# Kernel optimization log

Hardware: AMD Instinct MI355X
Metric: run time of the kernel (lower is better)

Reference implementation:

```python
import jax, jax.numpy as jnp
import numpy as np

N_NODES = 100000
N_EDGES = 3200000
IN_C, HID_C, OUT_C = 5, 128, 64


def setup_inputs() -> dict:
    key = jax.random.key(0)
    k_x, k_e, k_w1, k_b1, k_w2, k_b2 = jax.random.split(key, 6)
    x = jax.random.normal(k_x, (N_NODES, IN_C), dtype=jnp.float32)
    edge_index = jax.random.randint(k_e, (2, N_EDGES), 0, N_NODES, dtype=jnp.int32)
    # GCNConv learned params (glorot weights, zero-ish bias)
    W1 = jax.random.normal(k_w1, (IN_C, HID_C), dtype=jnp.float32) * (1.0 / np.sqrt(IN_C))
    b1 = jax.random.normal(k_b1, (HID_C,), dtype=jnp.float32) * 0.01
    W2 = jax.random.normal(k_w2, (HID_C, OUT_C), dtype=jnp.float32) * (1.0 / np.sqrt(HID_C))
    b2 = jax.random.normal(k_b2, (OUT_C,), dtype=jnp.float32) * 0.01
    return {"x": x, "edge_index": edge_index, "W1": W1, "b1": b1, "W2": W2, "b2": b2}


def _gcn_conv(x, src, dst, deg_inv_sqrt, W, b):
    """One GCNConv (PyG defaults: self-loops already in src/dst, symmetric norm, bias)."""
    h = x @ W                                   # [N, C_out]
    norm = deg_inv_sqrt[src] * deg_inv_sqrt[dst]  # [E+N]
    msg = h[src] * norm[:, None]                # gather + scale
    out = jax.ops.segment_sum(msg, dst, num_segments=x.shape[0])  # scatter-add
    return out + b


def reference(x, edge_index, W1, b1, W2, b2):
    n = x.shape[0]
    loop = jnp.arange(n, dtype=edge_index.dtype)
    src = jnp.concatenate([edge_index[0], loop])  # self-loops appended
    dst = jnp.concatenate([edge_index[1], loop])
    deg = jax.ops.segment_sum(jnp.ones_like(src, dtype=x.dtype), dst, num_segments=n)
    deg_inv_sqrt = jnp.where(deg > 0, jax.lax.rsqrt(deg), 0.0)
    h = _gcn_conv(x, src, dst, deg_inv_sqrt, W1, b1)
    z = _gcn_conv(h, src, dst, deg_inv_sqrt, W2, b2)
    return z
```

## Files before the change

### kernel.cpp

```cpp
#include <hip/hip_runtime.h>

#define IN_C  5
#define HID_C 128
#define OUT_C 64

#define KB   256
#define NBP  512
#define CAP  10240
#define TILE 4096
#define BTH  512
#define EPT  (TILE / BTH)
#define GNODES 64


__global__ void k_init(int* __restrict__ gcursor) {
    gcursor[threadIdx.x] = threadIdx.x * CAP;
}

__global__ __launch_bounds__(BTH) void k_bin(const int* __restrict__ src,
                                             const int* __restrict__ dstp,
                                             int* __restrict__ gcursor,
                                             int* __restrict__ binned, int e) {
    __shared__ int lhist[NBP];
    __shared__ int lfill[NBP];
    __shared__ int lgpos[NBP];
    int tid = threadIdx.x;
    int tbeg = blockIdx.x * TILE;
    for (int j = tid; j < NBP; j += BTH) { lhist[j] = 0; lfill[j] = 0; }
    __syncthreads();
    int pk[EPT], bk[EPT];
    #pragma unroll
    for (int q = 0; q < EPT; ++q) {
        int idx = tbeg + q * BTH + tid;
        if (idx < e) {
            int s = src[idx], d = dstp[idx];
            pk[q] = ((d & 255) << 24) | s;
            bk[q] = ((unsigned)d) >> 8;
            atomicAdd(&lhist[bk[q]], 1);
        } else bk[q] = -1;
    }
    __syncthreads();
    int hv = lhist[tid];
    if (hv > 0) lgpos[tid] = atomicAdd(&gcursor[tid], hv);
    __syncthreads();
    #pragma unroll
    for (int q = 0; q < EPT; ++q) {
        if (bk[q] >= 0) {
            int pos = lgpos[bk[q]] + atomicAdd(&lfill[bk[q]], 1);
            binned[pos] = pk[q];
        }
    }
}

__global__ __launch_bounds__(BTH) void k_build(int* __restrict__ binned,
                                               const int* __restrict__ gcursor,
                                               const float* __restrict__ x,
                                               int2* __restrict__ pse,
                                               float* __restrict__ xs, int n) {
    __shared__ int cnt[KB];
    __shared__ int wt[4];
    __shared__ int wte[4];
    __shared__ int stage[CAP];
    int tid = threadIdx.x;
    int lane = tid & 63, w = tid >> 6;
    int bkt = blockIdx.x;
    int beg = bkt * CAP;
    int tot = gcursor[bkt] - beg;
    if (tid < KB) cnt[tid] = 0;
    __syncthreads();
    int4 r[5];
    #pragma unroll
    for (int it = 0; it < 5; ++it) {
        int j0 = (tid << 2) + it * (BTH * 4);
        if (j0 < tot) {
            r[it] = *(const int4*)(binned + beg + j0);
            atomicAdd(&cnt[((unsigned)r[it].x) >> 24], 1);
            if (j0 + 1 < tot) atomicAdd(&cnt[((unsigned)r[it].y) >> 24], 1);
            if (j0 + 2 < tot) atomicAdd(&cnt[((unsigned)r[it].z) >> 24], 1);
            if (j0 + 3 < tot) atomicAdd(&cnt[((unsigned)r[it].w) >> 24], 1);
        }
    }
    __syncthreads();
    int deg = (tid < KB) ? cnt[tid] : 0;
    int v = deg;
    #pragma unroll
    for (int m = 1; m < 64; m <<= 1) { int u = __shfl_up(v, m); if (lane >= m) v += u; }
    if (tid < KB && lane == 63) wt[w] = v;
    __syncthreads();
    if (tid == 0) {
        int s = 0;
        #pragma unroll
        for (int k = 0; k < 4; ++k) { wte[k] = s; s += wt[k]; }
    }
    __syncthreads();
    if (tid < KB) {
        int rel = wte[w] + v - deg;
        int node = bkt * KB + tid;
        pse[node] = make_int2(beg + rel, beg + rel + deg);
        cnt[tid] = rel;
        float d = rsqrtf(1.0f + (float)deg);
        float4 q0 = {0, 0, 0, 0}, q1 = {0, 0, 0, 0};
        if (node < n) {
            q0.x = x[node * IN_C + 0] * d;
            q0.y = x[node * IN_C + 1] * d;
            q0.z = x[node * IN_C + 2] * d;
            q0.w = x[node * IN_C + 3] * d;
            q1.x = x[node * IN_C + 4] * d;
            q1.y = d;
        }
        ((float4*)(xs + (size_t)node * 8))[0] = q0;
        ((float4*)(xs + (size_t)node * 8))[1] = q1;
    }
    __syncthreads();
    #pragma unroll
    for (int it = 0; it < 5; ++it) {
        int j0 = (tid << 2) + it * (BTH * 4);
        if (j0 < tot) {
            {
                int slot = atomicAdd(&cnt[((unsigned)r[it].x) >> 24], 1);
                stage[slot] = r[it].x & 0xFFFFFF;
            }
            if (j0 + 1 < tot) {
                int slot = atomicAdd(&cnt[((unsigned)r[it].y) >> 24], 1);
                stage[slot] = r[it].y & 0xFFFFFF;
            }
            if (j0 + 2 < tot) {
                int slot = atomicAdd(&cnt[((unsigned)r[it].z) >> 24], 1);
                stage[slot] = r[it].z & 0xFFFFFF;
            }
            if (j0 + 3 < tot) {
                int slot = atomicAdd(&cnt[((unsigned)r[it].w) >> 24], 1);
                stage[slot] = r[it].w & 0xFFFFFF;
            }
        }
    }
    __syncthreads();
    for (int j = tid; j < tot; j += BTH)
        binned[beg + j] = stage[j];
}

__global__ __launch_bounds__(BTH) void k_gath0(const int* __restrict__ srclist,
                                               const int2* __restrict__ pse,
                                               const float* __restrict__ feat,
                                               float* __restrict__ outf,
                                               float* __restrict__ tout, int n) {
    int tid = threadIdx.x;
    int node = blockIdx.x * GNODES + (tid >> 3);
    int sub = tid & 7;
    if (node >= n) return;
    int2 pp = pse[node];
    int ps = pp.x, pe = pp.y;
    float a0 = 0, a1 = 0, a2 = 0, a3 = 0, a4 = 0, a5 = 0;
    int j = ps + sub;
    for (; j + 24 < pe; j += 32) {
        int s0 = srclist[j],      s1 = srclist[j + 8];
        int s2 = srclist[j + 16], s3 = srclist[j + 24];
        const float4* q0 = (const float4*)(feat + (size_t)s0 * 8);
        const float4* q1 = (const float4*)(feat + (size_t)s1 * 8);
        const float4* q2 = (const float4*)(feat + (size_t)s2 * 8);
        const float4* q3 = (const float4*)(feat + (size_t)s3 * 8);
        float4 rA0 = q0[0], rA1 = q0[1];
        float4 rB0 = q1[0], rB1 = q1[1];
        float4 rC0 = q2[0], rC1 = q2[1];
        float4 rD0 = q3[0], rD1 = q3[1];
        a0 += (rA0.x + rB0.x) + (rC0.x + rD0.x);
        a1 += (rA0.y + rB0.y) + (rC0.y + rD0.y);
        a2 += (rA0.z + rB0.z) + (rC0.z + rD0.z);
        a3 += (rA0.w + rB0.w) + (rC0.w + rD0.w);
        a4 += (rA1.x + rB1.x) + (rC1.x + rD1.x);
        a5 += (rA1.y + rB1.y) + (rC1.y + rD1.y);
    }
    for (; j < pe; j += 8) {
        int sA = srclist[j];
        const float4* qA = (const float4*)(feat + (size_t)sA * 8);
        float4 rA0 = qA[0], rA1 = qA[1];
        a0 += rA0.x; a1 += rA0.y; a2 += rA0.z; a3 += rA0.w; a4 += rA1.x;
        a5 += rA1.y;
    }
    #pragma unroll
    for (int m = 1; m < 8; m <<= 1) {
        a0 += __shfl_xor(a0, m);
        a1 += __shfl_xor(a1, m);
        a2 += __shfl_xor(a2, m);
        a3 += __shfl_xor(a3, m);
        a4 += __shfl_xor(a4, m);
        a5 += __shfl_xor(a5, m);
    }
    if (sub == 0) {
        const float4* psr = (const float4*)(feat + (size_t)node * 8);
        float4 s0 = psr[0], s1 = psr[1];
        float d = s1.y;
        a0 += s0.x; a1 += s0.y; a2 += s0.z; a3 += s0.w; a4 += s1.x;
        a5 += s1.y;
        float d2 = d * d;
        float4 o0, o1;
        o0.x = d2 * a0; o0.y = d2 * a1; o0.z = d2 * a2; o0.w = d2 * a3;
        o1.x = d2 * a4;
        o1.y = d;
        o1.z = 0.0f; o1.w = 0.0f;
        tout[node] = d * a5;
        ((float4*)(outf + (size_t)node * 8))[0] = o0;
        ((float4*)(outf + (size_t)node * 8))[1] = o1;
    }
}

__global__ __launch_bounds__(BTH) void k_gout(const int* __restrict__ srclist,
                                              const int2* __restrict__ pse,
                                              const float* __restrict__ feat,
                                              const float* __restrict__ t,
                                              const float* __restrict__ W1,
                                              const float* __restrict__ b1,
                                              const float* __restrict__ W2,
                                              const float* __restrict__ b2,
                                              float* __restrict__ out, int n) {
    __shared__ float snode[GNODES * 8];
    __shared__ float sW[IN_C * OUT_C + 2 * OUT_C];
    int tid = threadIdx.x;
    if (tid < IN_C * OUT_C) {
        int k = tid >> 6, c = tid & 63;
        float acc = 0.0f;
        for (int m = 0; m < HID_C; ++m)
            acc += W1[k * HID_C + m] * W2[m * OUT_C + c];
        sW[tid] = acc;
    } else if (tid < IN_C * OUT_C + OUT_C) {
        int c = tid - IN_C * OUT_C;
        float acc = 0.0f;
        for (int m = 0; m < HID_C; ++m)
            acc += b1[m] * W2[m * OUT_C + c];
        sW[tid] = acc;
    } else if (tid < IN_C * OUT_C + 2 * OUT_C) {
        sW[tid] = b2[tid - IN_C * OUT_C - OUT_C];
    }
    int node = blockIdx.x * GNODES + (tid >> 3);
    int sub = tid & 7;
    bool act = (node < n);
    float a0 = 0, a1 = 0, a2 = 0, a3 = 0, a4 = 0;
    if (act) {
        int2 pp = pse[node];
        int ps = pp.x, pe = pp.y;
        int j = ps + sub;
        for (; j + 24 < pe; j += 32) {
            int s0 = srclist[j],      s1 = srclist[j + 8];
            int s2 = srclist[j + 16], s3 = srclist[j + 24];
            const float4* q0 = (const float4*)(feat + (size_t)s0 * 8);
            const float4* q1 = (const float4*)(feat + (size_t)s1 * 8);
            const float4* q2 = (const float4*)(feat + (size_t)s2 * 8);
            const float4* q3 = (const float4*)(feat + (size_t)s3 * 8);
            float4 rA0 = q0[0], rA1 = q0[1];
            float4 rB0 = q1[0], rB1 = q1[1];
            float4 rC0 = q2[0], rC1 = q2[1];
            float4 rD0 = q3[0], rD1 = q3[1];
            a0 += (rA0.x + rB0.x) + (rC0.x + rD0.x);
            a1 += (rA0.y + rB0.y) + (rC0.y + rD0.y);
            a2 += (rA0.z + rB0.z) + (rC0.z + rD0.z);
            a3 += (rA0.w + rB0.w) + (rC0.w + rD0.w);
            a4 += (rA1.x + rB1.x) + (rC1.x + rD1.x);
        }
        for (; j < pe; j += 8) {
            int sA = srclist[j];
            const float4* qA = (const float4*)(feat + (size_t)sA * 8);
            float4 rA0 = qA[0], rA1 = qA[1];
            a0 += rA0.x; a1 += rA0.y; a2 += rA0.z; a3 += rA0.w; a4 += rA1.x;
        }
    }
    #pragma unroll
    for (int m = 1; m < 8; m <<= 1) {
        a0 += __shfl_xor(a0, m);
        a1 += __shfl_xor(a1, m);
        a2 += __shfl_xor(a2, m);
        a3 += __shfl_xor(a3, m);
        a4 += __shfl_xor(a4, m);
    }
    if (act && sub == 0) {
        const float4* psr = (const float4*)(feat + (size_t)node * 8);
        float4 s0 = psr[0], s1 = psr[1];
        float d = s1.y;
        a0 += s0.x; a1 += s0.y; a2 += s0.z; a3 += s0.w; a4 += s1.x;
        float* sn = snode + (tid >> 3) * 8;
        sn[0] = d * a0; sn[1] = d * a1; sn[2] = d * a2;
        sn[3] = d * a3; sn[4] = d * a4; sn[5] = t[node];
    }
    __syncthreads();
    int base = blockIdx.x * GNODES;
    for (int u = tid; u < GNODES * 16; u += BTH) {
        int ln = u >> 4, q = u & 15;
        int i = base + ln;
        if (i >= n) continue;
        const float* a = snode + ln * 8;
        float ti = a[5];
        float4 acc = ((const float4*)(sW + IN_C * OUT_C + OUT_C))[q];
        float4 bq  = ((const float4*)(sW + IN_C * OUT_C))[q];
        acc.x += ti * bq.x; acc.y += ti * bq.y;
        acc.z += ti * bq.z; acc.w += ti * bq.w;
        #pragma unroll
        for (int k = 0; k < IN_C; ++k) {
            float ak = a[k];
            float4 wk = ((const float4*)(sW + k * OUT_C))[q];
            acc.x += ak * wk.x; acc.y += ak * wk.y;
            acc.z += ak * wk.z; acc.w += ak * wk.w;
        }
        ((float4*)out)[(size_t)i * 16 + q] = acc;
    }
}

extern "C" void kernel_launch(void* const* d_in, const int* in_sizes, int n_in,
                              void* d_out, int out_size, void* d_ws, size_t ws_size,
                              hipStream_t stream) {
    const float* x   = (const float*)d_in[0];
    const int*   ei  = (const int*)d_in[1];
    const float* W1  = (const float*)d_in[2];
    const float* b1  = (const float*)d_in[3];
    const float* W2  = (const float*)d_in[4];
    const float* b2  = (const float*)d_in[5];
    float* out = (float*)d_out;

    const int n = in_sizes[0] / IN_C;
    const int e = in_sizes[1] / 2;
    const int* src = ei;
    const int* dst = ei + e;
    const int NB = (n + KB - 1) / KB;
    const int NKB = NB * KB;

    int*   gcursor = (int*)d_ws;
    int*   binned  = gcursor + 512;
    int2*  pse     = (int2*)(binned + (size_t)NBP * CAP);
    float* xs      = (float*)(pse + NKB);
    float* p1      = xs + (size_t)8 * NKB;
    float* t       = p1 + (size_t)8 * NKB;

    const int gB = (e + TILE - 1) / TILE;
    const int gG = (n + GNODES - 1) / GNODES;

    k_init  <<<1, 512, 0, stream>>>(gcursor);
    k_bin   <<<gB, BTH, 0, stream>>>(src, dst, gcursor, binned, e);
    k_build <<<NB, BTH, 0, stream>>>(binned, gcursor, x, pse, xs, n);
    k_gath0 <<<gG, BTH, 0, stream>>>(binned, pse, xs, p1, t, n);
    k_gout  <<<gG, BTH, 0, stream>>>(binned, pse, p1, t,
                                     W1, b1, W2, b2, out, n);
}
```

Baseline: 190.4 us.

## Locally sort binned edges in LDS for coalesced writes; trim gather loads

k_bin now does a block-level exclusive scan of its bucket histogram and stages edges sorted by bucket in shared memory, then writes them out in runs so each bucket's global writes are contiguous instead of scattered. k_build drops its 40KB staging buffer and scatters directly into the global bucket segment in place. The gather kernels load only the float2 or float that is actually used rather than a full second float4, and the init kernel becomes a memset with cursor offsets folded into k_bin. The in-place scatter in k_build relies on every block reading its segment into registers before writing, and the extra LDS in k_bin (about 40KB) may lower its occupancy.

```diff
diff --git a/kernel.cpp b/kernel.cpp
--- a/kernel.cpp
+++ b/kernel.cpp
@@ -13,20 +13,22 @@
 #define GNODES 64
 
 
-__global__ void k_init(int* __restrict__ gcursor) {
-    gcursor[threadIdx.x] = threadIdx.x * CAP;
-}
-
 __global__ __launch_bounds__(BTH) void k_bin(const int* __restrict__ src,
                                              const int* __restrict__ dstp,
                                              int* __restrict__ gcursor,
                                              int* __restrict__ binned, int e) {
     __shared__ int lhist[NBP];
     __shared__ int lfill[NBP];
-    __shared__ int lgpos[NBP];
+    __shared__ int lgofs[NBP];
+    __shared__ int lbeg[NBP];
+    __shared__ int lsort[TILE];
+    __shared__ int gdst[TILE];
+    __shared__ int wsum[8];
+    __shared__ int stot;
     int tid = threadIdx.x;
+    int lane = tid & 63, w = tid >> 6;
     int tbeg = blockIdx.x * TILE;
-    for (int j = tid; j < NBP; j += BTH) { lhist[j] = 0; lfill[j] = 0; }
+    lhist[tid] = 0; lfill[tid] = 0;
     __syncthreads();
     int pk[EPT], bk[EPT];
     #pragma unroll
@@ -40,16 +42,36 @@
         } else bk[q] = -1;
     }
     __syncthreads();
-    int hv = lhist[tid];
-    if (hv > 0) lgpos[tid] = atomicAdd(&gcursor[tid], hv);
+    int h = lhist[tid];
+    int v = h;
+    #pragma unroll
+    for (int m = 1; m < 64; m <<= 1) { int u = __shfl_up(v, m); if (lane >= m) v += u; }
+    if (lane == 63) wsum[w] = v;
+    __syncthreads();
+    if (tid == 0) {
+        int s = 0;
+        #pragma unroll
+        for (int k = 0; k < 8; ++k) { int tv = wsum[k]; wsum[k] = s; s += tv; }
+    }
+    __syncthreads();
+    int excl = wsum[w] + v - h;
+    lbeg[tid] = excl;
+    if (h > 0)
+        lgofs[tid] = tid * CAP + atomicAdd(&gcursor[tid], h) - excl;
+    if (tid == BTH - 1) stot = excl + h;
     __syncthreads();
     #pragma unroll
     for (int q = 0; q < EPT; ++q) {
         if (bk[q] >= 0) {
-            int pos = lgpos[bk[q]] + atomicAdd(&lfill[bk[q]], 1);
-            binned[pos] = pk[q];
-        }
-    }
+            int slot = lbeg[bk[q]] + atomicAdd(&lfill[bk[q]], 1);
+            lsort[slot] = pk[q];
+            gdst[slot] = lgofs[bk[q]] + slot;
+        }
+    }
+    __syncthreads();
+    int tot = stot;
+    for (int i = tid; i < tot; i += BTH)
+        binned[gdst[i]] = lsort[i];
 }
 
 __global__ __launch_bounds__(BTH) void k_build(int* __restrict__ binned,
@@ -60,12 +82,11 @@
     __shared__ int cnt[KB];
     __shared__ int wt[4];
     __shared__ int wte[4];
-    __shared__ int stage[CAP];
     int tid = threadIdx.x;
     int lane = tid & 63, w = tid >> 6;
     int bkt = blockIdx.x;
     int beg = bkt * CAP;
-    int tot = gcursor[bkt] - beg;
+    int tot = gcursor[bkt];
     if (tid < KB) cnt[tid] = 0;
     __syncthreads();
     int4 r[5];
@@ -118,25 +139,22 @@
         if (j0 < tot) {
             {
                 int slot = atomicAdd(&cnt[((unsigned)r[it].x) >> 24], 1);
-                stage[slot] = r[it].x & 0xFFFFFF;
+                binned[beg + slot] = r[it].x & 0xFFFFFF;
             }
             if (j0 + 1 < tot) {
                 int slot = atomicAdd(&cnt[((unsigned)r[it].y) >> 24], 1);
-                stage[slot] = r[it].y & 0xFFFFFF;
+                binned[beg + slot] = r[it].y & 0xFFFFFF;
             }
             if (j0 + 2 < tot) {
                 int slot = atomicAdd(&cnt[((unsigned)r[it].z) >> 24], 1);
-                stage[slot] = r[it].z & 0xFFFFFF;
+                binned[beg + slot] = r[it].z & 0xFFFFFF;
             }
             if (j0 + 3 < tot) {
                 int slot = atomicAdd(&cnt[((unsigned)r[it].w) >> 24], 1);
-                stage[slot] = r[it].w & 0xFFFFFF;
+                binned[beg + slot] = r[it].w & 0xFFFFFF;
             }
         }
     }
-    __syncthreads();
-    for (int j = tid; j < tot; j += BTH)
-        binned[beg + j] = stage[j];
 }
 
 __global__ __launch_bounds__(BTH) void k_gath0(const int* __restrict__ srclist,
@@ -155,14 +173,14 @@
     for (; j + 24 < pe; j += 32) {
         int s0 = srclist[j],      s1 = srclist[j + 8];
         int s2 = srclist[j + 16], s3 = srclist[j + 24];
-        const float4* q0 = (const float4*)(feat + (size_t)s0 * 8);
-        const float4* q1 = (const float4*)(feat + (size_t)s1 * 8);
-        const float4* q2 = (const float4*)(feat + (size_t)s2 * 8);
-        const float4* q3 = (const float4*)(feat + (size_t)s3 * 8);
-        float4 rA0 = q0[0], rA1 = q0[1];
-        float4 rB0 = q1[0], rB1 = q1[1];
-        float4 rC0 = q2[0], rC1 = q2[1];
-        float4 rD0 = q3[0], rD1 = q3[1];
+        const float* b0 = feat + (size_t)s0 * 8;
+        const float* b1 = feat + (size_t)s1 * 8;
+        const float* b2 = feat + (size_t)s2 * 8;
+        const float* b3 = feat + (size_t)s3 * 8;
+        float4 rA0 = *(const float4*)b0; float2 rA1 = *(const float2*)(b0 + 4);
+        float4 rB0 = *(const float4*)b1; float2 rB1 = *(const float2*)(b1 + 4);
+        float4 rC0 = *(const float4*)b2; float2 rC1 = *(const float2*)(b2 + 4);
+        float4 rD0 = *(const float4*)b3; float2 rD1 = *(const float2*)(b3 + 4);
         a0 += (rA0.x + rB0.x) + (rC0.x + rD0.x);
         a1 += (rA0.y + rB0.y) + (rC0.y + rD0.y);
         a2 += (rA0.z + rB0.z) + (rC0.z + rD0.z);
@@ -172,10 +190,10 @@
     }
     for (; j < pe; j += 8) {
         int sA = srclist[j];
-        const float4* qA = (const float4*)(feat + (size_t)sA * 8);
-        float4 rA0 = qA[0], rA1 = qA[1];
-        a0 += rA0.x; a1 += rA0.y; a2 += rA0.z; a3 += rA0.w; a4 += rA1.x;
-        a5 += rA1.y;
+        const float* bA = feat + (size_t)sA * 8;
+        float4 rA0 = *(const float4*)bA; float2 rA1 = *(const float2*)(bA + 4);
+        a0 += rA0.x; a1 += rA0.y; a2 += rA0.z; a3 += rA0.w;
+        a4 += rA1.x; a5 += rA1.y;
     }
     #pragma unroll
     for (int m = 1; m < 8; m <<= 1) {
@@ -242,25 +260,25 @@
         for (; j + 24 < pe; j += 32) {
             int s0 = srclist[j],      s1 = srclist[j + 8];
             int s2 = srclist[j + 16], s3 = srclist[j + 24];
-            const float4* q0 = (const float4*)(feat + (size_t)s0 * 8);
-            const float4* q1 = (const float4*)(feat + (size_t)s1 * 8);
-            const float4* q2 = (const float4*)(feat + (size_t)s2 * 8);
-            const float4* q3 = (const float4*)(feat + (size_t)s3 * 8);
-            float4 rA0 = q0[0], rA1 = q0[1];
-            float4 rB0 = q1[0], rB1 = q1[1];
-            float4 rC0 = q2[0], rC1 = q2[1];
-            float4 rD0 = q3[0], rD1 = q3[1];
+            const float* c0 = feat + (size_t)s0 * 8;
+            const float* c1 = feat + (size_t)s1 * 8;
+            const float* c2 = feat + (size_t)s2 * 8;
+            const float* c3 = feat + (size_t)s3 * 8;
+            float4 rA0 = *(const float4*)c0; float rA4 = c0[4];
+            float4 rB0 = *(const float4*)c1; float rB4 = c1[4];
+            float4 rC0 = *(const float4*)c2; float rC4 = c2[4];
+            float4 rD0 = *(const float4*)c3; float rD4 = c3[4];
             a0 += (rA0.x + rB0.x) + (rC0.x + rD0.x);
             a1 += (rA0.y + rB0.y) + (rC0.y + rD0.y);
             a2 += (rA0.z + rB0.z) + (rC0.z + rD0.z);
             a3 += (rA0.w + rB0.w) + (rC0.w + rD0.w);
-            a4 += (rA1.x + rB1.x) + (rC1.x + rD1.x);
+            a4 += (rA4 + rB4) + (rC4 + rD4);
         }
         for (; j < pe; j += 8) {
             int sA = srclist[j];
-            const float4* qA = (const float4*)(feat + (size_t)sA * 8);
-            float4 rA0 = qA[0], rA1 = qA[1];
-            a0 += rA0.x; a1 += rA0.y; a2 += rA0.z; a3 += rA0.w; a4 += rA1.x;
+            const float* cA = feat + (size_t)sA * 8;
+            float4 rA0 = *(const float4*)cA;
+            a0 += rA0.x; a1 += rA0.y; a2 += rA0.z; a3 += rA0.w; a4 += cA[4];
         }
     }
     #pragma unroll
@@ -331,7 +349,7 @@
     const int gB = (e + TILE - 1) / TILE;
     const int gG = (n + GNODES - 1) / GNODES;
 
-    k_init  <<<1, 512, 0, stream>>>(gcursor);
+    hipMemsetAsync(gcursor, 0, NBP * sizeof(int), stream);
     k_bin   <<<gB, BTH, 0, stream>>>(src, dst, gcursor, binned, e);
     k_build <<<NB, BTH, 0, stream>>>(binned, gcursor, x, pse, xs, n);
     k_gath0 <<<gG, BTH, 0, stream>>>(binned, pse, xs, p1, t, n);
```

After: 198.3 us. +4.1%, slower.
